# Optimization experiments

Hardware: AMD Instinct MI355X
Metric: run time of the kernel (lower is better)

## Reference

```python
import jax, jax.numpy as jnp
import numpy as np

N_QUBITS = 8
DEPTH = 2
INPUT_DIM = 64
HIDDEN_DIM = 8
SEQ_LEN = 128
BATCH = 512
DIM = 2 ** N_QUBITS


def _build_perm():
    """Compose the depth*n CNOT ring (CNOT(i,(i+1)%n) for i in range(n), repeated DEPTH times)
    into a single basis-state permutation. Wire 0 is the most-significant qubit (torchquantum order).
    CNOT is an involution on basis states: new[s] = old[f(s)], f flips target bit iff control bit set.
    Sequential composition: perm <- perm[f_j]."""
    n = N_QUBITS
    perm = np.arange(DIM)
    for _ in range(DEPTH):
        for c in range(n):
            t = (c + 1) % n
            s = np.arange(DIM)
            cbit = (s >> (n - 1 - c)) & 1
            fs = np.where(cbit == 1, s ^ (1 << (n - 1 - t)), s)
            perm = perm[fs]
    return jnp.asarray(perm, dtype=jnp.int32)


def _build_signs():
    s = np.arange(DIM)[:, None]
    w = np.arange(N_QUBITS)[None, :]
    bits = (s >> (N_QUBITS - 1 - w)) & 1
    return jnp.asarray(1.0 - 2.0 * bits, dtype=jnp.float32)  # [DIM, n]


PERM = _build_perm()
SIGNS = _build_signs()


def _qlayer(ang):
    """QLayer: RX(ang_i) on wire i of |0...0> (encoder RX + trainable RX fused since RX(a)RX(b)=RX(a+b)),
    then DEPTH CNOT-ring layers (precomputed permutation), then PauliZ expectation per wire.
    ang: [B, n] -> returns [B, n]."""
    half = 0.5 * ang
    v0 = jnp.cos(half).astype(jnp.complex64)          # [B, n]
    v1 = (-1j) * jnp.sin(half).astype(jnp.complex64)  # RX|0> = cos(t/2)|0> - i sin(t/2)|1>
    vecs = jnp.stack([v0, v1], axis=-1)               # [B, n, 2]
    b = ang.shape[0]
    state = jnp.ones((b, 1), jnp.complex64)
    for w in range(N_QUBITS):  # build product state, wire 0 most significant
        state = (state[:, :, None] * vecs[:, w, None, :]).reshape(b, -1)
    state = state[:, PERM]  # apply composed CNOT entanglers
    probs = jnp.real(state * jnp.conj(state)).astype(jnp.float32)  # [B, 2^n]
    return probs @ SIGNS  # [B, n] PauliZ expectations


def setup_inputs() -> dict:
    key = jax.random.key(0)
    ks = jax.random.split(key, 14)
    d = {"inputs": jax.random.normal(ks[0], (SEQ_LEN, BATCH, INPUT_DIM), jnp.float32)}
    fan_in = INPUT_DIM + HIDDEN_DIM
    scale = 1.0 / np.sqrt(fan_in)
    names = ["f", "i", "u", "o"]
    for j, nm in enumerate(names):
        d[f"W_{nm}"] = jax.random.uniform(ks[1 + 3 * j], (N_QUBITS, fan_in), jnp.float32, -scale, scale)
        d[f"b_{nm}"] = jax.random.uniform(ks[2 + 3 * j], (N_QUBITS,), jnp.float32, -scale, scale)
        d[f"th_{nm}"] = jax.random.normal(ks[3 + 3 * j], (N_QUBITS,), jnp.float32) * 0.1
    return d


def reference(inputs, W_f, b_f, W_i, b_i, W_u, b_u, W_o, b_o, th_f, th_i, th_u, th_o):
    batch = inputs.shape[1]

    def step(carry, x):
        hx, cx = carry
        comb = jnp.concatenate([x, hx], axis=1)  # [B, input+hidden]
        f = jax.nn.sigmoid(_qlayer(comb @ W_f.T + b_f + th_f))
        i = jax.nn.sigmoid(_qlayer(comb @ W_i.T + b_i + th_i))
        g = jnp.tanh(_qlayer(comb @ W_u.T + b_u + th_u))
        o = jax.nn.sigmoid(_qlayer(comb @ W_o.T + b_o + th_o))
        cx = f * cx + i * g
        hx = o * jnp.tanh(cx)
        return (hx, cx), hx

    init = (jnp.zeros((batch, HIDDEN_DIM), jnp.float32), jnp.zeros((batch, HIDDEN_DIM), jnp.float32))
    (hx, cx), outputs = jax.lax.scan(step, init, inputs)
    return (outputs, (hx, cx))
```

## Files before the change

kernel.cpp:

```cpp
#include <hip/hip_runtime.h>
#include <cstdint>
#include <cstddef>


constexpr int SEQ    = 128;
constexpr int NBATCH = 512;
constexpr int INDIM  = 64;
constexpr int FANIN  = 72;
constexpr long OUT_HX = (long)SEQ * NBATCH * 8;
constexpr long OUT_CX = OUT_HX + (long)NBATCH * 8;

#define SWZ(v, imm) __int_as_float(__builtin_amdgcn_ds_swizzle(__float_as_int(v), (imm)))

__device__ __forceinline__ float fast_cos(float ang) {
    const float rev = ang * 0.15915494309189535f;
    return __builtin_amdgcn_cosf(__builtin_amdgcn_fractf(rev));
}

__global__ __launch_bounds__(256) void xproj_kernel(
    const float* __restrict__ x,
    const float* __restrict__ Wf, const float* __restrict__ bf, const float* __restrict__ thf,
    const float* __restrict__ Wi, const float* __restrict__ bi, const float* __restrict__ thi,
    const float* __restrict__ Wu, const float* __restrict__ bu, const float* __restrict__ thu,
    const float* __restrict__ Wo, const float* __restrict__ bo, const float* __restrict__ tho,
    float* __restrict__ xp)
{
    __shared__ float lx[128 * 68];
    __shared__ float lbias[32];
    const int tid = threadIdx.x;
    const long rowBase = (long)blockIdx.x * 128;

    if (tid < 32) {
        const int g = tid >> 3, w = tid & 7;
        const float* bg = (g == 0) ? bf : (g == 1) ? bi : (g == 2) ? bu : bo;
        const float* tg = (g == 0) ? thf : (g == 1) ? thi : (g == 2) ? thu : tho;
        lbias[tid] = bg[w] + tg[w];
    }

    const float4* xin = reinterpret_cast<const float4*>(x + rowBase * INDIM);
#pragma unroll
    for (int i = 0; i < 8; ++i) {
        const int f   = i * 256 + tid;
        const int row = f >> 4;
        const int kq  = f & 15;
        *reinterpret_cast<float4*>(&lx[row * 68 + kq * 4]) = xin[f];
    }
    __syncthreads();

    const int og = tid & 3;
    const int q  = tid >> 2;
    const float* Wg = (og == 0) ? Wf : (og == 1) ? Wi : (og == 2) ? Wu : Wo;

    float acc[2][8];
#pragma unroll
    for (int r = 0; r < 2; ++r)
#pragma unroll
        for (int j = 0; j < 8; ++j) acc[r][j] = 0.f;

#pragma unroll
    for (int k4 = 0; k4 < 16; ++k4) {
        const float4 x0 = *reinterpret_cast<const float4*>(&lx[q * 68 + k4 * 4]);
        const float4 x1 = *reinterpret_cast<const float4*>(&lx[(q + 64) * 68 + k4 * 4]);
#pragma unroll
        for (int j = 0; j < 8; ++j) {
            const float4 wv = *reinterpret_cast<const float4*>(Wg + j * FANIN + k4 * 4);
            acc[0][j] = fmaf(x0.x, wv.x, acc[0][j]);
            acc[0][j] = fmaf(x0.y, wv.y, acc[0][j]);
            acc[0][j] = fmaf(x0.z, wv.z, acc[0][j]);
            acc[0][j] = fmaf(x0.w, wv.w, acc[0][j]);
            acc[1][j] = fmaf(x1.x, wv.x, acc[1][j]);
            acc[1][j] = fmaf(x1.y, wv.y, acc[1][j]);
            acc[1][j] = fmaf(x1.z, wv.z, acc[1][j]);
            acc[1][j] = fmaf(x1.w, wv.w, acc[1][j]);
        }
    }

#pragma unroll
    for (int r = 0; r < 2; ++r) {
        float4 o0, o1;
        o0.x = acc[r][0] + lbias[og * 8 + 0];
        o0.y = acc[r][1] + lbias[og * 8 + 1];
        o0.z = acc[r][2] + lbias[og * 8 + 2];
        o0.w = acc[r][3] + lbias[og * 8 + 3];
        o1.x = acc[r][4] + lbias[og * 8 + 4];
        o1.y = acc[r][5] + lbias[og * 8 + 5];
        o1.z = acc[r][6] + lbias[og * 8 + 6];
        o1.w = acc[r][7] + lbias[og * 8 + 7];
        float* dst = xp + (rowBase + q + 64 * r) * 32 + og * 8;
        reinterpret_cast<float4*>(dst)[0] = o0;
        reinterpret_cast<float4*>(dst)[1] = o1;
    }
}

template <bool FUSED>
__global__ __launch_bounds__(256) void qlstm_scan_kernel(
    const float* __restrict__ x,
    const float* __restrict__ xp,
    const float* __restrict__ Wf, const float* __restrict__ bf, const float* __restrict__ thf,
    const float* __restrict__ Wi, const float* __restrict__ bi, const float* __restrict__ thi,
    const float* __restrict__ Wu, const float* __restrict__ bu, const float* __restrict__ thu,
    const float* __restrict__ Wo, const float* __restrict__ bo, const float* __restrict__ tho,
    float* __restrict__ out)
{
    const int tid  = threadIdx.x;
    const int lane = tid & 31;
    const int row  = (blockIdx.x << 3) + (tid >> 5);
    const int g    = lane >> 3;
    const int w    = lane & 7;

    const float* Wg = (g == 0) ? Wf : (g == 1) ? Wi : (g == 2) ? Wu : Wo;

    float wh0, wh1, wh2, wh3, wh4, wh5, wh6, wh7;
    {
        const float4* p = reinterpret_cast<const float4*>(Wg + w * FANIN + 64);
        const float4 a = p[0], b4 = p[1];
        wh0 = a.x; wh1 = a.y; wh2 = a.z; wh3 = a.w;
        wh4 = b4.x; wh5 = b4.y; wh6 = b4.z; wh7 = b4.w;
    }

    float bias = 0.f;
    float wx[64];
    if constexpr (FUSED) {
        const float* bg = (g == 0) ? bf : (g == 1) ? bi : (g == 2) ? bu : bo;
        const float* tg = (g == 0) ? thf : (g == 1) ? thi : (g == 2) ? thu : tho;
        bias = bg[w] + tg[w];
#pragma unroll
        for (int k4 = 0; k4 < 16; ++k4) {
            const float4 v = reinterpret_cast<const float4*>(Wg + w * FANIN)[k4];
            wx[4 * k4 + 0] = v.x; wx[4 * k4 + 1] = v.y;
            wx[4 * k4 + 2] = v.z; wx[4 * k4 + 3] = v.w;
        }
    }

    const unsigned mask = (unsigned)((0x55AAD5EAF5FAFDABull >> (w * 8)) & 0xFFull);

    const bool  isU = (g == 2);
    const float ZL  = isU ? -2.0f : -1.0f;
    const float A   = isU ?  2.0f :  1.0f;
    const float B   = isU ? -1.0f :  0.0f;

    float h0 = 0.f, h1 = 0.f, h2 = 0.f, h3 = 0.f, h4 = 0.f, h5 = 0.f, h6 = 0.f, h7 = 0.f;
    float cxl = 0.f;
    float nhx = 0.f;

    float xv0 = 0.f, xv1 = 0.f;
    if constexpr (!FUSED) {
        xv0 = xp[(long)row * 32 + lane];
        xv1 = xp[((long)NBATCH + row) * 32 + lane];
    }

    for (int t = 0; t < SEQ; ++t) {
        float xv2 = 0.f;
        if constexpr (!FUSED) {
            if (t + 2 < SEQ) xv2 = xp[((long)(t + 2) * NBATCH + row) * 32 + lane];
        }

        float ang;
        if constexpr (FUSED) {
            const float4* xr4 = reinterpret_cast<const float4*>(x + ((long)t * NBATCH + row) * INDIM);
            float acc = bias;
#pragma unroll
            for (int k4 = 0; k4 < 16; ++k4) {
                const float4 v = xr4[k4];
                acc = fmaf(v.x, wx[4 * k4 + 0], acc);
                acc = fmaf(v.y, wx[4 * k4 + 1], acc);
                acc = fmaf(v.z, wx[4 * k4 + 2], acc);
                acc = fmaf(v.w, wx[4 * k4 + 3], acc);
            }
            ang = acc;
        } else {
            ang = xv0;
        }

        const float d0 = fmaf(h0, wh0, fmaf(h1, wh1, fmaf(h2, wh2, h3 * wh3)));
        const float d1 = fmaf(h4, wh4, fmaf(h5, wh5, fmaf(h6, wh6, h7 * wh7)));
        ang += d0 + d1;

        const float c = fast_cos(ang);

        const float cb0 = SWZ(c, 0x018);
        const float cb1 = SWZ(c, 0x038);
        const float cb2 = SWZ(c, 0x058);
        const float cb3 = SWZ(c, 0x078);
        const float cb4 = SWZ(c, 0x098);
        const float cb5 = SWZ(c, 0x0B8);
        const float cb6 = SWZ(c, 0x0D8);
        const float cb7 = SWZ(c, 0x0F8);

        const float p0 = (mask & 0x01u) ? cb0 : 1.0f;
        const float p1 = (mask & 0x02u) ? cb1 : 1.0f;
        const float p2 = (mask & 0x04u) ? cb2 : 1.0f;
        const float p3 = (mask & 0x08u) ? cb3 : 1.0f;
        const float p4 = (mask & 0x10u) ? cb4 : 1.0f;
        const float p5 = (mask & 0x20u) ? cb5 : 1.0f;
        const float p6 = (mask & 0x40u) ? cb6 : 1.0f;
        const float p7 = (mask & 0x80u) ? cb7 : 1.0f;
        const float z = ((p0 * p1) * (p2 * p3)) * ((p4 * p5) * (p6 * p7));

        const float e   = __expf(z * ZL);
        const float s   = __builtin_amdgcn_rcpf(1.0f + e);
        const float act = fmaf(A, s, B);

        const float fg = SWZ(act, 0x007);
        const float ig = SWZ(act, 0x107);
        const float ug = SWZ(act, 0x207);
        const float og = SWZ(act, 0x307);

        const float ncx = fmaf(fg, cxl, ig * ug);
        const float et  = __expf(-2.0f * ncx);
        const float tc  = fmaf(2.0f, __builtin_amdgcn_rcpf(1.0f + et), -1.0f);
        nhx = og * tc;
        cxl = ncx;

        if (lane < 8) out[((long)t * NBATCH + row) * 8 + lane] = nhx;

        h0 = SWZ(nhx, 0x000);
        h1 = SWZ(nhx, 0x020);
        h2 = SWZ(nhx, 0x040);
        h3 = SWZ(nhx, 0x060);
        h4 = SWZ(nhx, 0x080);
        h5 = SWZ(nhx, 0x0A0);
        h6 = SWZ(nhx, 0x0C0);
        h7 = SWZ(nhx, 0x0E0);

        if constexpr (!FUSED) { xv0 = xv1; xv1 = xv2; }
    }

    if (lane < 8) {
        out[OUT_HX + (long)row * 8 + lane] = nhx;
        out[OUT_CX + (long)row * 8 + lane] = cxl;
    }
}

extern "C" void kernel_launch(void* const* d_in, const int* in_sizes, int n_in,
                              void* d_out, int out_size, void* d_ws, size_t ws_size,
                              hipStream_t stream)
{
    const float* x = (const float*)d_in[0];

    const float *Wf, *bf, *thf, *Wi, *bi, *thi, *Wu, *bu, *thu, *Wo, *bo, *tho;
    if (in_sizes[3] == 8) {
        Wf = (const float*)d_in[1];  bf = (const float*)d_in[2];  thf = (const float*)d_in[3];
        Wi = (const float*)d_in[4];  bi = (const float*)d_in[5];  thi = (const float*)d_in[6];
        Wu = (const float*)d_in[7];  bu = (const float*)d_in[8];  thu = (const float*)d_in[9];
        Wo = (const float*)d_in[10]; bo = (const float*)d_in[11]; tho = (const float*)d_in[12];
    } else {
        Wf = (const float*)d_in[1];  bf = (const float*)d_in[2];
        Wi = (const float*)d_in[3];  bi = (const float*)d_in[4];
        Wu = (const float*)d_in[5];  bu = (const float*)d_in[6];
        Wo = (const float*)d_in[7];  bo = (const float*)d_in[8];
        thf = (const float*)d_in[9]; thi = (const float*)d_in[10];
        thu = (const float*)d_in[11]; tho = (const float*)d_in[12];
    }

    float* out = (float*)d_out;
    float* xp  = (float*)d_ws;
    const size_t need = (size_t)SEQ * NBATCH * 32 * sizeof(float);

    if (ws_size >= need) {
        xproj_kernel<<<(SEQ * NBATCH) / 128, 256, 0, stream>>>(
            x, Wf, bf, thf, Wi, bi, thi, Wu, bu, thu, Wo, bo, tho, xp);
        qlstm_scan_kernel<false><<<NBATCH / 8, 256, 0, stream>>>(
            x, xp, Wf, bf, thf, Wi, bi, thi, Wu, bu, thu, Wo, bo, tho, out);
    } else {
        qlstm_scan_kernel<true><<<NBATCH / 8, 256, 0, stream>>>(
            x, nullptr, Wf, bf, thf, Wi, bi, thi, Wu, bu, thu, Wo, bo, tho, out);
    }
}
```

Baseline: 159.7 us.

## Remap scan-kernel lanes so cross-lane broadcasts use DPP instead of ds_swizzle

```diff
diff --git a/kernel.cpp b/kernel.cpp
--- a/kernel.cpp
+++ b/kernel.cpp
@@ -16,6 +16,15 @@
     const float rev = ang * 0.15915494309189535f;
     return __builtin_amdgcn_cosf(__builtin_amdgcn_fractf(rev));
 }
+
+template <int CTRL> __device__ __forceinline__ float DPPF(float x) {
+    return __int_as_float(__builtin_amdgcn_update_dpp(
+        0, __float_as_int(x), CTRL, 0xF, 0xF, false));
+}
+__device__ __forceinline__ float xlane1(float x) { return DPPF<0xB1>(x); }
+__device__ __forceinline__ float xlane2(float x) { return DPPF<0x4E>(x); }
+__device__ __forceinline__ float xlane4(float x) { return DPPF<0x141>(DPPF<0x1B>(x)); }
+__device__ __forceinline__ float xlane8(float x) { return DPPF<0x128>(x); }
 
 __global__ __launch_bounds__(256) void xproj_kernel(
     const float* __restrict__ x,
@@ -92,10 +101,114 @@
     }
 }
 
-template <bool FUSED>
 __global__ __launch_bounds__(256) void qlstm_scan_kernel(
+    const float* __restrict__ xp,
+    const float* __restrict__ Wf, const float* __restrict__ Wi,
+    const float* __restrict__ Wu, const float* __restrict__ Wo,
+    float* __restrict__ out)
+{
+    const int tid  = threadIdx.x;
+    const int lane = tid & 31;
+    const int row  = (blockIdx.x << 3) + (tid >> 5);
+    const int g    = (lane & 1) | ((lane >> 3) & 2);
+    const int w    = (lane >> 1) & 7;
+
+    const float* Wg = (g == 0) ? Wf : (g == 1) ? Wi : (g == 2) ? Wu : Wo;
+
+    float whx[8];
+#pragma unroll
+    for (int d = 0; d < 8; ++d) whx[d] = Wg[w * FANIN + 64 + (w ^ d)];
+
+    const unsigned mask = (unsigned)((0x55AAD5EAF5FAFDABull >> (w * 8)) & 0xFFull);
+    bool pm[8];
+#pragma unroll
+    for (int d = 0; d < 8; ++d) pm[d] = ((mask >> (w ^ d)) & 1u) != 0u;
+
+    const bool  isU  = (g == 2);
+    const float ZL   = isU ? -2.0f : -1.0f;
+    const float A    = isU ?  2.0f :  1.0f;
+    const float B    = isU ? -1.0f :  0.0f;
+    const bool  gOdd = (lane & 1) != 0;
+    const bool  gHi  = (lane & 16) != 0;
+
+    const int col = g * 8 + w;
+
+    float hh0=0.f,hh1=0.f,hh2=0.f,hh3=0.f,hh4=0.f,hh5=0.f,hh6=0.f,hh7=0.f;
+    float cxl = 0.f;
+
+    float xv0 = xp[(long)row * 32 + col];
+    float xv1 = xp[((long)NBATCH + row) * 32 + col];
+
+    for (int t = 0; t < SEQ; ++t) {
+        float xv2 = 0.f;
+        if (t + 2 < SEQ) xv2 = xp[((long)(t + 2) * NBATCH + row) * 32 + col];
+
+        const float d0 = fmaf(hh0, whx[0], fmaf(hh1, whx[1], fmaf(hh2, whx[2], hh3 * whx[3])));
+        const float d1 = fmaf(hh4, whx[4], fmaf(hh5, whx[5], fmaf(hh6, whx[6], hh7 * whx[7])));
+        const float ang = xv0 + d0 + d1;
+
+        const float c = fast_cos(ang);
+
+        const float cc0 = c;
+        const float cc1 = xlane2(cc0);
+        const float cc2 = xlane4(cc0);
+        const float cc3 = xlane4(cc1);
+        const float cc4 = xlane8(cc0);
+        const float cc5 = xlane8(cc1);
+        const float cc6 = xlane8(cc2);
+        const float cc7 = xlane8(cc3);
+
+        const float p0 = pm[0] ? cc0 : 1.0f;
+        const float p1 = pm[1] ? cc1 : 1.0f;
+        const float p2 = pm[2] ? cc2 : 1.0f;
+        const float p3 = pm[3] ? cc3 : 1.0f;
+        const float p4 = pm[4] ? cc4 : 1.0f;
+        const float p5 = pm[5] ? cc5 : 1.0f;
+        const float p6 = pm[6] ? cc6 : 1.0f;
+        const float p7 = pm[7] ? cc7 : 1.0f;
+        const float z = ((p0 * p1) * (p2 * p3)) * ((p4 * p5) * (p6 * p7));
+
+        const float e   = __expf(z * ZL);
+        const float act = fmaf(A, __builtin_amdgcn_rcpf(1.0f + e), B);
+
+        const float a01 = xlane1(act);
+        const float ae  = gOdd ? a01 : act;
+        const float ao  = gOdd ? act : a01;
+        const float be  = SWZ(ae, 0x401F);
+        const float bo  = SWZ(ao, 0x401F);
+        const float fg  = gHi ? be : ae;
+        const float ig  = gHi ? bo : ao;
+        const float ug  = gHi ? ae : be;
+        const float og  = gHi ? ao : bo;
+
+        const float ncx = fmaf(fg, cxl, ig * ug);
+        const float et  = __expf(-2.0f * ncx);
+        const float tc  = fmaf(2.0f, __builtin_amdgcn_rcpf(1.0f + et), -1.0f);
+        const float nhx = og * tc;
+        cxl = ncx;
+
+        if ((lane & 0x11) == 0) out[((long)t * NBATCH + row) * 8 + w] = nhx;
+
+        hh0 = nhx;
+        hh1 = xlane2(hh0);
+        hh2 = xlane4(hh0);
+        hh3 = xlane4(hh1);
+        hh4 = xlane8(hh0);
+        hh5 = xlane8(hh1);
+        hh6 = xlane8(hh2);
+        hh7 = xlane8(hh3);
+
+        xv0 = xv1; xv1 = xv2;
+    }
+
+    if ((lane & 0x11) == 0) {
+        out[OUT_HX + (long)row * 8 + w] = hh0;
+        out[OUT_CX + (long)row * 8 + w] = cxl;
+    }
+}
+
+__global__ __launch_bounds__(256) void qlstm_scan_fused(
     const float* __restrict__ x,
-    const float* __restrict__ xp,
     const float* __restrict__ Wf, const float* __restrict__ bf, const float* __restrict__ thf,
     const float* __restrict__ Wi, const float* __restrict__ bi, const float* __restrict__ thi,
     const float* __restrict__ Wu, const float* __restrict__ bu, const float* __restrict__ thu,
@@ -109,6 +222,8 @@
     const int w    = lane & 7;
 
     const float* Wg = (g == 0) ? Wf : (g == 1) ? Wi : (g == 2) ? Wu : Wo;
+    const float* bg = (g == 0) ? bf : (g == 1) ? bi : (g == 2) ? bu : bo;
+    const float* tg = (g == 0) ? thf : (g == 1) ? thi : (g == 2) ? thu : tho;
 
     float wh0, wh1, wh2, wh3, wh4, wh5, wh6, wh7;
     {
@@ -117,75 +232,42 @@
         wh0 = a.x; wh1 = a.y; wh2 = a.z; wh3 = a.w;
         wh4 = b4.x; wh5 = b4.y; wh6 = b4.z; wh7 = b4.w;
     }
-
-    float bias = 0.f;
+    const float bias = bg[w] + tg[w];
     float wx[64];
-    if constexpr (FUSED) {
-        const float* bg = (g == 0) ? bf : (g == 1) ? bi : (g == 2) ? bu : bo;
-        const float* tg = (g == 0) ? thf : (g == 1) ? thi : (g == 2) ? thu : tho;
-        bias = bg[w] + tg[w];
-#pragma unroll
-        for (int k4 = 0; k4 < 16; ++k4) {
-            const float4 v = reinterpret_cast<const float4*>(Wg + w * FANIN)[k4];
-            wx[4 * k4 + 0] = v.x; wx[4 * k4 + 1] = v.y;
-            wx[4 * k4 + 2] = v.z; wx[4 * k4 + 3] = v.w;
-        }
+#pragma unroll
+    for (int k4 = 0; k4 < 16; ++k4) {
+        const float4 v = reinterpret_cast<const float4*>(Wg + w * FANIN)[k4];
+        wx[4*k4+0] = v.x; wx[4*k4+1] = v.y; wx[4*k4+2] = v.z; wx[4*k4+3] = v.w;
     }
 
     const unsigned mask = (unsigned)((0x55AAD5EAF5FAFDABull >> (w * 8)) & 0xFFull);
-
     const bool  isU = (g == 2);
     const float ZL  = isU ? -2.0f : -1.0f;
     const float A   = isU ?  2.0f :  1.0f;
     const float B   = isU ? -1.0f :  0.0f;
 
-    float h0 = 0.f, h1 = 0.f, h2 = 0.f, h3 = 0.f, h4 = 0.f, h5 = 0.f, h6 = 0.f, h7 = 0.f;
-    float cxl = 0.f;
-    float nhx = 0.f;
-
-    float xv0 = 0.f, xv1 = 0.f;
-    if constexpr (!FUSED) {
-        xv0 = xp[(long)row * 32 + lane];
-        xv1 = xp[((long)NBATCH + row) * 32 + lane];
-    }
+    float h0=0,h1=0,h2=0,h3=0,h4=0,h5=0,h6=0,h7=0, cxl=0, nhx=0;
 
     for (int t = 0; t < SEQ; ++t) {
-        float xv2 = 0.f;
-        if constexpr (!FUSED) {
-            if (t + 2 < SEQ) xv2 = xp[((long)(t + 2) * NBATCH + row) * 32 + lane];
+        const float4* xr4 = reinterpret_cast<const float4*>(x + ((long)t * NBATCH + row) * INDIM);
+        float acc = bias;
+#pragma unroll
+        for (int k4 = 0; k4 < 16; ++k4) {
+            const float4 v = xr4[k4];
+            acc = fmaf(v.x, wx[4*k4+0], acc);
+            acc = fmaf(v.y, wx[4*k4+1], acc);
+            acc = fmaf(v.z, wx[4*k4+2], acc);
+            acc = fmaf(v.w, wx[4*k4+3], acc);
         }
-
-        float ang;
-        if constexpr (FUSED) {
-            const float4* xr4 = reinterpret_cast<const float4*>(x + ((long)t * NBATCH + row) * INDIM);
-            float acc = bias;
-#pragma unroll
-            for (int k4 = 0; k4 < 16; ++k4) {
-                const float4 v = xr4[k4];
-                acc = fmaf(v.x, wx[4 * k4 + 0], acc);
-                acc = fmaf(v.y, wx[4 * k4 + 1], acc);
-                acc = fmaf(v.z, wx[4 * k4 + 2], acc);
-                acc = fmaf(v.w, wx[4 * k4 + 3], acc);
-            }
-            ang = acc;
-        } else {
-            ang = xv0;
-        }
-
-        const float d0 = fmaf(h0, wh0, fmaf(h1, wh1, fmaf(h2, wh2, h3 * wh3)));
-        const float d1 = fmaf(h4, wh4, fmaf(h5, wh5, fmaf(h6, wh6, h7 * wh7)));
-        ang += d0 + d1;
+        float ang = acc;
+        ang += fmaf(h0, wh0, fmaf(h1, wh1, fmaf(h2, wh2, h3 * wh3)))
+             + fmaf(h4, wh4, fmaf(h5, wh5, fmaf(h6, wh6, h7 * wh7)));
 
         const float c = fast_cos(ang);
-
-        const float cb0 = SWZ(c, 0x018);
-        const float cb1 = SWZ(c, 0x038);
-        const float cb2 = SWZ(c, 0x058);
-        const float cb3 = SWZ(c, 0x078);
-        const float cb4 = SWZ(c, 0x098);
-        const float cb5 = SWZ(c, 0x0B8);
-        const float cb6 = SWZ(c, 0x0D8);
-        const float cb7 = SWZ(c, 0x0F8);
+        const float cb0 = SWZ(c, 0x018); const float cb1 = SWZ(c, 0x038);
+        const float cb2 = SWZ(c, 0x058); const float cb3 = SWZ(c, 0x078);
+        const float cb4 = SWZ(c, 0x098); const float cb5 = SWZ(c, 0x0B8);
+        const float cb6 = SWZ(c, 0x0D8); const float cb7 = SWZ(c, 0x0F8);
 
         const float p0 = (mask & 0x01u) ? cb0 : 1.0f;
         const float p1 = (mask & 0x02u) ? cb1 : 1.0f;
@@ -195,11 +277,10 @@
         const float p5 = (mask & 0x20u) ? cb5 : 1.0f;
         const float p6 = (mask & 0x40u) ? cb6 : 1.0f;
         const float p7 = (mask & 0x80u) ? cb7 : 1.0f;
-        const float z = ((p0 * p1) * (p2 * p3)) * ((p4 * p5) * (p6 * p7));
+        const float z = ((p0*p1)*(p2*p3)) * ((p4*p5)*(p6*p7));
 
         const float e   = __expf(z * ZL);
-        const float s   = __builtin_amdgcn_rcpf(1.0f + e);
-        const float act = fmaf(A, s, B);
+        const float act = fmaf(A, __builtin_amdgcn_rcpf(1.0f + e), B);
 
         const float fg = SWZ(act, 0x007);
         const float ig = SWZ(act, 0x107);
@@ -214,16 +295,10 @@
 
         if (lane < 8) out[((long)t * NBATCH + row) * 8 + lane] = nhx;
 
-        h0 = SWZ(nhx, 0x000);
-        h1 = SWZ(nhx, 0x020);
-        h2 = SWZ(nhx, 0x040);
-        h3 = SWZ(nhx, 0x060);
-        h4 = SWZ(nhx, 0x080);
-        h5 = SWZ(nhx, 0x0A0);
-        h6 = SWZ(nhx, 0x0C0);
-        h7 = SWZ(nhx, 0x0E0);
-
-        if constexpr (!FUSED) { xv0 = xv1; xv1 = xv2; }
+        h0 = SWZ(nhx, 0x000); h1 = SWZ(nhx, 0x020);
+        h2 = SWZ(nhx, 0x040); h3 = SWZ(nhx, 0x060);
+        h4 = SWZ(nhx, 0x080); h5 = SWZ(nhx, 0x0A0);
+        h6 = SWZ(nhx, 0x0C0); h7 = SWZ(nhx, 0x0E0);
     }
 
     if (lane < 8) {
@@ -260,10 +335,10 @@
     if (ws_size >= need) {
         xproj_kernel<<<(SEQ * NBATCH) / 128, 256, 0, stream>>>(
             x, Wf, bf, thf, Wi, bi, thi, Wu, bu, thu, Wo, bo, tho, xp);
-        qlstm_scan_kernel<false><<<NBATCH / 8, 256, 0, stream>>>(
-            x, xp, Wf, bf, thf, Wi, bi, thi, Wu, bu, thu, Wo, bo, tho, out);
+        qlstm_scan_kernel<<<NBATCH / 8, 256, 0, stream>>>(
+            xp, Wf, Wi, Wu, Wo, out);
     } else {
-        qlstm_scan_kernel<true><<<NBATCH / 8, 256, 0, stream>>>(
-            x, nullptr, Wf, bf, thf, Wi, bi, thi, Wu, bu, thu, Wo, bo, tho, out);
-    }
-}
+        qlstm_scan_fused<<<NBATCH / 8, 256, 0, stream>>>(
+            x, Wf, bf, thf, Wi, bi, thi, Wu, bu, thu, Wo, bo, tho, out);
+    }
+}
```

Measured after the change: 163.7 us. 1.03x slower.
